# Kernel tuning notes

Measured on AMD Instinct MI355X. Metric: run time of the kernel, lower is better.

## Reference

```python
import jax, jax.numpy as jnp
import numpy as np

B, N, C, H = 32, 384, 768, 12
EPS = 1e-6

def setup_inputs() -> dict:
    key = jax.random.key(0)
    k0, k1, k2, k3 = jax.random.split(key, 4)
    x = jax.random.normal(k0, (B, N, C), dtype=jnp.float32)
    # binary keep-mask over key tokens, broadcastable to [B,1,N,N]
    policy = (jax.random.uniform(k1, (B, 1, 1, N)) > 0.5).astype(jnp.float32)
    qkv_w = jax.random.normal(k2, (3 * C, C), dtype=jnp.float32) * 0.02
    qkv_b = jnp.zeros((3 * C,), dtype=jnp.float32)
    proj_w = jax.random.normal(k3, (C, C), dtype=jnp.float32) * 0.02
    proj_b = jnp.zeros((C,), dtype=jnp.float32)
    return {"x": x, "policy": policy, "qkv_w": qkv_w, "qkv_b": qkv_b,
            "proj_w": proj_w, "proj_b": proj_b}

def reference(x, policy, qkv_w, qkv_b, proj_w, proj_b):
    b, n, c = x.shape
    hd = c // H
    scale = hd ** -0.5
    qkv = (x @ qkv_w.T + qkv_b).reshape(b, n, 3, H, hd).transpose(2, 0, 3, 1, 4)
    q, k, v = qkv[0], qkv[1], qkv[2]
    attn = jnp.einsum('bhnd,bhmd->bhnm', q, k) * scale  # [B,H,N,N]
    # softmax_with_policy: eye-blend so every token attends to itself,
    # then eps-regularized masked softmax
    eye = jnp.eye(n, dtype=policy.dtype)[None, None]  # [1,1,N,N]
    attn_policy = policy + (1.0 - policy) * eye       # broadcast -> [B,1,N,N]
    max_att = attn.max(axis=-1, keepdims=True)
    e = jnp.exp(attn - max_att) * attn_policy
    attn = (e + EPS / n) / (e.sum(axis=-1, keepdims=True) + EPS)
    out = jnp.einsum('bhnm,bhmd->bnhd', attn, v).reshape(b, n, c)
    return out @ proj_w.T + proj_b
```

## Files before the change

kernel.cpp:

```cpp
#include <hip/hip_runtime.h>

#define BB 32
#define NN 384
#define CC 768
#define HH 12
#define HD 64

typedef __attribute__((ext_vector_type(4))) float f32x4;
typedef __attribute__((ext_vector_type(8))) __bf16 bf16x8;
typedef __attribute__((ext_vector_type(4))) __bf16 bf16x4;

static __device__ __forceinline__ f32x4 mfma16(bf16x8 a, bf16x8 b, f32x4 c) {
    return __builtin_amdgcn_mfma_f32_16x16x32_bf16(a, b, c, 0, 0, 0);
}

__global__ void cvt_kernel(const float* __restrict__ src, __bf16* __restrict__ dst,
                           int n8, float scale) {
    int i = blockIdx.x * blockDim.x + threadIdx.x;
    if (i >= n8) return;
    f32x4 a = *(const f32x4*)(src + (size_t)i * 8);
    f32x4 b = *(const f32x4*)(src + (size_t)i * 8 + 4);
    bf16x8 o;
#pragma unroll
    for (int j = 0; j < 4; ++j) { o[j] = (__bf16)(a[j] * scale); o[j + 4] = (__bf16)(b[j] * scale); }
    *(bf16x8*)(dst + (size_t)i * 8) = o;
}

template <int EPI>
__global__ __launch_bounds__(256, 2) void gemm_kernel(
    const __bf16* __restrict__ A, const __bf16* __restrict__ Bw,
    const float* __restrict__ bias,
    __bf16* __restrict__ qkbuf, __bf16* __restrict__ vtbuf,
    float* __restrict__ fout) {
    __shared__ __bf16 Alds[128][72];
    __shared__ __bf16 Blds[128][72];

    const int tid = threadIdx.x;
    const int l = tid & 63;
    const int w = tid >> 6;
    const int g = l >> 4, q16 = l & 15;
    const int mb = blockIdx.x * 128;
    const int nb = blockIdx.y * 128;
    const int wrb = (w >> 1) * 64;
    const int wcb = (w & 1) * 64;
    const int srow = tid >> 3;
    const int sc8 = (tid & 7) * 8;

    const __bf16* Ab = A + (size_t)mb * CC;
    const __bf16* Bb = Bw + (size_t)nb * CC;

    f32x4 acc[4][4] = {};
    bf16x8 sa[4], sb[4];

#pragma unroll
    for (int p = 0; p < 4; ++p) {
        sa[p] = *(const bf16x8*)&Ab[(size_t)(p * 32 + srow) * CC + sc8];
        sb[p] = *(const bf16x8*)&Bb[(size_t)(p * 32 + srow) * CC + sc8];
    }

    for (int kt = 0; kt < 12; ++kt) {
#pragma unroll
        for (int p = 0; p < 4; ++p) {
            *(bf16x8*)&Alds[p * 32 + srow][sc8] = sa[p];
            *(bf16x8*)&Blds[p * 32 + srow][sc8] = sb[p];
        }
        __syncthreads();
        if (kt < 11) {
            const int kn = (kt + 1) * 64 + sc8;
#pragma unroll
            for (int p = 0; p < 4; ++p) {
                sa[p] = *(const bf16x8*)&Ab[(size_t)(p * 32 + srow) * CC + kn];
                sb[p] = *(const bf16x8*)&Bb[(size_t)(p * 32 + srow) * CC + kn];
            }
        }
#pragma unroll
        for (int c = 0; c < 2; ++c) {
            bf16x8 af[4], bf_[4];
#pragma unroll
            for (int m = 0; m < 4; ++m)
                af[m] = *(const bf16x8*)&Alds[wrb + m * 16 + q16][c * 32 + g * 8];
#pragma unroll
            for (int n = 0; n < 4; ++n)
                bf_[n] = *(const bf16x8*)&Blds[wcb + n * 16 + q16][c * 32 + g * 8];
#pragma unroll
            for (int m = 0; m < 4; ++m)
#pragma unroll
                for (int n = 0; n < 4; ++n)
                    acc[m][n] = mfma16(af[m], bf_[n], acc[m][n]);
        }
        __syncthreads();
    }

    if constexpr (EPI == 0) {
        const int bbatch = mb / NN;
        const int tokb = mb % NN;
#pragma unroll
        for (int n = 0; n < 4; ++n) {
            const int colb = nb + wcb + n * 16;
            const int col = colb + q16;
            float bs = bias[col];
            if (colb < 2 * CC) {
                if (colb < CC) bs *= 0.125f;
#pragma unroll
                for (int m = 0; m < 4; ++m) {
                    const int row = mb + wrb + m * 16 + g * 4;
#pragma unroll
                    for (int r = 0; r < 4; ++r)
                        qkbuf[(size_t)(row + r) * 1536 + col] = (__bf16)(acc[m][n][r] + bs);
                }
            } else {
                const int dd = (col - 2 * CC) & 63;
                const int hh = (colb - 2 * CC) >> 6;
                __bf16* vp = vtbuf + ((size_t)(bbatch * HH + hh) * HD + dd) * NN;
#pragma unroll
                for (int m = 0; m < 4; ++m) {
                    const int tok = tokb + wrb + m * 16 + g * 4;
                    bf16x4 pk;
#pragma unroll
                    for (int r = 0; r < 4; ++r) pk[r] = (__bf16)(acc[m][n][r] + bs);
                    *(bf16x4*)&vp[tok] = pk;
                }
            }
        }
    } else {
#pragma unroll
        for (int n = 0; n < 4; ++n) {
            const int col = nb + wcb + n * 16 + q16;
            const float bs = bias[col];
#pragma unroll
            for (int m = 0; m < 4; ++m)
#pragma unroll
                for (int r = 0; r < 4; ++r)
                    fout[(size_t)(mb + wrb + m * 16 + g * 4 + r) * CC + col] = acc[m][n][r] + bs;
        }
    }
}

__global__ __launch_bounds__(512, 2) void attn_kernel(
    const __bf16* __restrict__ qkbuf, const __bf16* __restrict__ vtbuf,
    const float* __restrict__ policy, __bf16* __restrict__ attb) {
    __shared__ __bf16 Klds[NN][72];
    __shared__ __bf16 Vlds[HD][NN + 8];
    __shared__ float pol[NN];

    const int tid = threadIdx.x;
    const int l = tid & 63;
    const int w = tid >> 6;
    const int g = l >> 4, q16 = l & 15;
    const int qblk = blockIdx.x;
    const int h = blockIdx.y;
    const int b = blockIdx.z;

    if (tid < NN) pol[tid] = policy[b * NN + tid];

    const __bf16* kg = qkbuf + (size_t)b * NN * 1536 + CC + h * HD;
#pragma unroll
    for (int p = 0; p < 6; ++p) {
        const int s = p * 512 + tid;
        const int row = s >> 3, c8 = (s & 7) * 8;
        *(bf16x8*)&Klds[row][c8] = *(const bf16x8*)&kg[(size_t)row * 1536 + c8];
    }
    const __bf16* vg = vtbuf + (size_t)(b * HH + h) * HD * NN;
#pragma unroll
    for (int p = 0; p < 6; ++p) {
        const int s = p * 512 + tid;
        const int d = s / 48, tk = (s % 48) * 8;
        *(bf16x8*)&Vlds[d][tk] = *(const bf16x8*)&vg[(size_t)s * 8];
    }
    __syncthreads();

    const int qrow = qblk * 128 + w * 16 + q16;
    const __bf16* qg = qkbuf + ((size_t)b * NN + qrow) * 1536 + h * HD;
    bf16x8 qf0 = *(const bf16x8*)&qg[g * 8];
    bf16x8 qf1 = *(const bf16x8*)&qg[32 + g * 8];

    f32x4 st[24];
#pragma unroll
    for (int t = 0; t < 24; ++t) {
        bf16x8 k0 = *(const bf16x8*)&Klds[t * 16 + q16][g * 8];
        bf16x8 k1 = *(const bf16x8*)&Klds[t * 16 + q16][32 + g * 8];
        f32x4 z = {0.f, 0.f, 0.f, 0.f};
        st[t] = mfma16(k1, qf1, mfma16(k0, qf0, z));
    }

    float mx = -1e30f;
#pragma unroll
    for (int t = 0; t < 24; ++t)
#pragma unroll
        for (int r = 0; r < 4; ++r) mx = fmaxf(mx, st[t][r]);
    mx = fmaxf(mx, __shfl_xor(mx, 16));
    mx = fmaxf(mx, __shfl_xor(mx, 32));

    float sum = 0.f;
#pragma unroll
    for (int t = 0; t < 24; ++t) {
#pragma unroll
        for (int r = 0; r < 4; ++r) {
            const int key = t * 16 + g * 4 + r;
            const bool keep = (pol[key] > 0.5f) || (key == qrow);
            const float e = keep ? __expf(st[t][r] - mx) : 0.f;
            st[t][r] = e;
            sum += e;
        }
    }
    sum += __shfl_xor(sum, 16);
    sum += __shfl_xor(sum, 32);
    const float dinv = 1.f / (sum + 1e-6f);

    f32x4 oacc[4] = {};
#pragma unroll
    for (int c = 0; c < 12; ++c) {
        bf16x8 pf;
#pragma unroll
        for (int r = 0; r < 4; ++r) {
            pf[r] = (__bf16)st[2 * c][r];
            pf[r + 4] = (__bf16)st[2 * c + 1][r];
        }
#pragma unroll
        for (int db = 0; db < 4; ++db) {
            bf16x4 v0 = *(const bf16x4*)&Vlds[db * 16 + q16][c * 32 + g * 4];
            bf16x4 v1 = *(const bf16x4*)&Vlds[db * 16 + q16][c * 32 + 16 + g * 4];
            bf16x8 vf;
#pragma unroll
            for (int r = 0; r < 4; ++r) { vf[r] = v0[r]; vf[r + 4] = v1[r]; }
            oacc[db] = mfma16(vf, pf, oacc[db]);
        }
    }

    __bf16* op = attb + ((size_t)b * NN + qrow) * CC + h * HD;
#pragma unroll
    for (int db = 0; db < 4; ++db) {
        bf16x4 pk;
#pragma unroll
        for (int r = 0; r < 4; ++r) pk[r] = (__bf16)(oacc[db][r] * dinv);
        *(bf16x4*)&op[db * 16 + g * 4] = pk;
    }
}

extern "C" void kernel_launch(void* const* d_in, const int* in_sizes, int n_in,
                              void* d_out, int out_size, void* d_ws, size_t ws_size,
                              hipStream_t stream) {
    (void)in_sizes; (void)n_in; (void)out_size; (void)ws_size;
    const float* x      = (const float*)d_in[0];
    const float* policy = (const float*)d_in[1];
    const float* qkv_w  = (const float*)d_in[2];
    const float* qkv_b  = (const float*)d_in[3];
    const float* proj_w = (const float*)d_in[4];
    const float* proj_b = (const float*)d_in[5];
    float* out = (float*)d_out;

    __bf16* xb    = (__bf16*)d_ws;
    __bf16* wqkv  = xb + (size_t)12288 * 768;
    __bf16* wproj = wqkv + (size_t)2304 * 768;
    __bf16* qkbuf = wproj + (size_t)768 * 768;
    __bf16* vtbuf = qkbuf + (size_t)12288 * 1536;
    __bf16* attb  = vtbuf + (size_t)BB * HH * HD * NN;

    auto cvt = [&](const float* s, __bf16* d, size_t n, float sc) {
        const int n8 = (int)(n / 8);
        cvt_kernel<<<(n8 + 255) / 256, 256, 0, stream>>>(s, d, n8, sc);
    };
    cvt(x, xb, (size_t)12288 * 768, 1.f);
    cvt(qkv_w, wqkv, (size_t)768 * 768, 0.125f);
    cvt(qkv_w + (size_t)768 * 768, wqkv + (size_t)768 * 768, (size_t)1536 * 768, 1.f);
    cvt(proj_w, wproj, (size_t)768 * 768, 1.f);

    gemm_kernel<0><<<dim3(96, 18), 256, 0, stream>>>(xb, wqkv, qkv_b, qkbuf, vtbuf, nullptr);
    attn_kernel<<<dim3(3, HH, BB), 512, 0, stream>>>(qkbuf, vtbuf, policy, attb);
    gemm_kernel<1><<<dim3(96, 6), 256, 0, stream>>>(attb, wproj, proj_b, nullptr, nullptr, out);
}
```

Before: 155.1 us.

## Use direct global-to-LDS loads in GEMM and attention, read K from global

The GEMM now stages A/B tiles with global_load_lds straight into unpadded LDS. This drops the register prefetch double-buffering and raises the occupancy hint to 3. The attention kernel uses 256-thread blocks over 64 query rows, loads V into XOR-swizzled LDS via global_load_lds, reads K directly from global memory instead of LDS, and raises wave priority around the MFMA loops. The goal is to cut LDS footprint and staging instructions to raise occupancy. The cost is losing the global-load/compute overlap in the GEMM and adding repeated K reads from global/L2. Unpadded GEMM LDS rows may cause bank conflicts.

```diff
diff --git a/kernel.cpp b/kernel.cpp
--- a/kernel.cpp
+++ b/kernel.cpp
@@ -12,6 +12,11 @@
 
 static __device__ __forceinline__ f32x4 mfma16(bf16x8 a, bf16x8 b, f32x4 c) {
     return __builtin_amdgcn_mfma_f32_16x16x32_bf16(a, b, c, 0, 0, 0);
+}
+
+static __device__ __forceinline__ void gload_lds16(const void* g, void* l) {
+    __builtin_amdgcn_global_load_lds((const __attribute__((address_space(1))) void*)g,
+                                     (__attribute__((address_space(3))) void*)l, 16, 0, 0);
 }
 
 __global__ void cvt_kernel(const float* __restrict__ src, __bf16* __restrict__ dst,
@@ -27,13 +32,13 @@
 }
 
 template <int EPI>
-__global__ __launch_bounds__(256, 2) void gemm_kernel(
+__global__ __launch_bounds__(256, 3) void gemm_kernel(
     const __bf16* __restrict__ A, const __bf16* __restrict__ Bw,
     const float* __restrict__ bias,
     __bf16* __restrict__ qkbuf, __bf16* __restrict__ vtbuf,
     float* __restrict__ fout) {
-    __shared__ __bf16 Alds[128][72];
-    __shared__ __bf16 Blds[128][72];
+    __shared__ __bf16 Alds[128 * 64];
+    __shared__ __bf16 Blds[128 * 64];
 
     const int tid = threadIdx.x;
     const int l = tid & 63;
@@ -43,50 +48,34 @@
     const int nb = blockIdx.y * 128;
     const int wrb = (w >> 1) * 64;
     const int wcb = (w & 1) * 64;
-    const int srow = tid >> 3;
-    const int sc8 = (tid & 7) * 8;
-
-    const __bf16* Ab = A + (size_t)mb * CC;
-    const __bf16* Bb = Bw + (size_t)nb * CC;
+
+    const int srow = w * 8 + (l >> 3);
+    const int scol = (l & 7) * 8;
 
     f32x4 acc[4][4] = {};
-    bf16x8 sa[4], sb[4];
-
-#pragma unroll
-    for (int p = 0; p < 4; ++p) {
-        sa[p] = *(const bf16x8*)&Ab[(size_t)(p * 32 + srow) * CC + sc8];
-        sb[p] = *(const bf16x8*)&Bb[(size_t)(p * 32 + srow) * CC + sc8];
-    }
 
     for (int kt = 0; kt < 12; ++kt) {
-#pragma unroll
-        for (int p = 0; p < 4; ++p) {
-            *(bf16x8*)&Alds[p * 32 + srow][sc8] = sa[p];
-            *(bf16x8*)&Blds[p * 32 + srow][sc8] = sb[p];
+        const int kof = kt * 64 + scol;
+#pragma unroll
+        for (int i = 0; i < 4; ++i) {
+            gload_lds16(&A[(size_t)(mb + i * 32 + srow) * CC + kof], &Alds[i * 2048 + w * 512]);
+            gload_lds16(&Bw[(size_t)(nb + i * 32 + srow) * CC + kof], &Blds[i * 2048 + w * 512]);
         }
         __syncthreads();
-        if (kt < 11) {
-            const int kn = (kt + 1) * 64 + sc8;
-#pragma unroll
-            for (int p = 0; p < 4; ++p) {
-                sa[p] = *(const bf16x8*)&Ab[(size_t)(p * 32 + srow) * CC + kn];
-                sb[p] = *(const bf16x8*)&Bb[(size_t)(p * 32 + srow) * CC + kn];
-            }
-        }
 #pragma unroll
         for (int c = 0; c < 2; ++c) {
-            bf16x8 af[4], bf_[4];
+            bf16x8 af[4], bfr[4];
 #pragma unroll
             for (int m = 0; m < 4; ++m)
-                af[m] = *(const bf16x8*)&Alds[wrb + m * 16 + q16][c * 32 + g * 8];
+                af[m] = *(const bf16x8*)&Alds[(wrb + m * 16 + q16) * 64 + c * 32 + g * 8];
 #pragma unroll
             for (int n = 0; n < 4; ++n)
-                bf_[n] = *(const bf16x8*)&Blds[wcb + n * 16 + q16][c * 32 + g * 8];
+                bfr[n] = *(const bf16x8*)&Blds[(wcb + n * 16 + q16) * 64 + c * 32 + g * 8];
 #pragma unroll
             for (int m = 0; m < 4; ++m)
 #pragma unroll
                 for (int n = 0; n < 4; ++n)
-                    acc[m][n] = mfma16(af[m], bf_[n], acc[m][n]);
+                    acc[m][n] = mfma16(af[m], bfr[n], acc[m][n]);
         }
         __syncthreads();
     }
@@ -136,11 +125,10 @@
     }
 }
 
-__global__ __launch_bounds__(512, 2) void attn_kernel(
+__global__ __launch_bounds__(256, 3) void attn_kernel(
     const __bf16* __restrict__ qkbuf, const __bf16* __restrict__ vtbuf,
     const float* __restrict__ policy, __bf16* __restrict__ attb) {
-    __shared__ __bf16 Klds[NN][72];
-    __shared__ __bf16 Vlds[HD][NN + 8];
+    __shared__ __bf16 Vlds[HD * NN];
     __shared__ float pol[NN];
 
     const int tid = threadIdx.x;
@@ -151,37 +139,34 @@
     const int h = blockIdx.y;
     const int b = blockIdx.z;
 
-    if (tid < NN) pol[tid] = policy[b * NN + tid];
-
-    const __bf16* kg = qkbuf + (size_t)b * NN * 1536 + CC + h * HD;
-#pragma unroll
-    for (int p = 0; p < 6; ++p) {
-        const int s = p * 512 + tid;
-        const int row = s >> 3, c8 = (s & 7) * 8;
-        *(bf16x8*)&Klds[row][c8] = *(const bf16x8*)&kg[(size_t)row * 1536 + c8];
-    }
     const __bf16* vg = vtbuf + (size_t)(b * HH + h) * HD * NN;
 #pragma unroll
-    for (int p = 0; p < 6; ++p) {
-        const int s = p * 512 + tid;
-        const int d = s / 48, tk = (s % 48) * 8;
-        *(bf16x8*)&Vlds[d][tk] = *(const bf16x8*)&vg[(size_t)s * 8];
-    }
-    __syncthreads();
-
-    const int qrow = qblk * 128 + w * 16 + q16;
+    for (int p = 0; p < 12; ++p) {
+        const int cs = p * 256 + w * 64 + l;
+        const int row = cs / 48, cin = cs - row * 48;
+        gload_lds16(&vg[row * NN + ((cin ^ (row & 7)) << 3)], &Vlds[(p * 256 + w * 64) * 8]);
+    }
+    for (int i = tid; i < NN; i += 256) pol[i] = policy[b * NN + i];
+
+    const int qrow = qblk * 64 + w * 16 + q16;
     const __bf16* qg = qkbuf + ((size_t)b * NN + qrow) * 1536 + h * HD;
     bf16x8 qf0 = *(const bf16x8*)&qg[g * 8];
     bf16x8 qf1 = *(const bf16x8*)&qg[32 + g * 8];
 
+    const __bf16* kg = qkbuf + (size_t)b * NN * 1536 + CC + h * HD;
     f32x4 st[24];
+    __builtin_amdgcn_s_setprio(1);
 #pragma unroll
     for (int t = 0; t < 24; ++t) {
-        bf16x8 k0 = *(const bf16x8*)&Klds[t * 16 + q16][g * 8];
-        bf16x8 k1 = *(const bf16x8*)&Klds[t * 16 + q16][32 + g * 8];
+        const __bf16* kr = &kg[(size_t)(t * 16 + q16) * 1536 + g * 8];
+        bf16x8 k0 = *(const bf16x8*)kr;
+        bf16x8 k1 = *(const bf16x8*)(kr + 32);
         f32x4 z = {0.f, 0.f, 0.f, 0.f};
         st[t] = mfma16(k1, qf1, mfma16(k0, qf0, z));
     }
+    __builtin_amdgcn_s_setprio(0);
+
+    __syncthreads();
 
     float mx = -1e30f;
 #pragma unroll
@@ -208,6 +193,7 @@
     const float dinv = 1.f / (sum + 1e-6f);
 
     f32x4 oacc[4] = {};
+    __builtin_amdgcn_s_setprio(1);
 #pragma unroll
     for (int c = 0; c < 12; ++c) {
         bf16x8 pf;
@@ -218,14 +204,18 @@
         }
 #pragma unroll
         for (int db = 0; db < 4; ++db) {
-            bf16x4 v0 = *(const bf16x4*)&Vlds[db * 16 + q16][c * 32 + g * 4];
-            bf16x4 v1 = *(const bf16x4*)&Vlds[db * 16 + q16][c * 32 + 16 + g * 4];
+            const int row = db * 16 + q16;
+            const int sw = (row & 7) << 4;
+            const int byte0 = (row * NN + c * 32 + g * 4) * 2;
+            bf16x4 v0 = *(const bf16x4*)((const char*)Vlds + (byte0 ^ sw));
+            bf16x4 v1 = *(const bf16x4*)((const char*)Vlds + ((byte0 + 32) ^ sw));
             bf16x8 vf;
 #pragma unroll
             for (int r = 0; r < 4; ++r) { vf[r] = v0[r]; vf[r + 4] = v1[r]; }
             oacc[db] = mfma16(vf, pf, oacc[db]);
         }
     }
+    __builtin_amdgcn_s_setprio(0);
 
     __bf16* op = attb + ((size_t)b * NN + qrow) * CC + h * HD;
 #pragma unroll
@@ -266,6 +256,6 @@
     cvt(proj_w, wproj, (size_t)768 * 768, 1.f);
 
     gemm_kernel<0><<<dim3(96, 18), 256, 0, stream>>>(xb, wqkv, qkv_b, qkbuf, vtbuf, nullptr);
-    attn_kernel<<<dim3(3, HH, BB), 512, 0, stream>>>(qkbuf, vtbuf, policy, attb);
+    attn_kernel<<<dim3(6, HH, BB), 256, 0, stream>>>(qkbuf, vtbuf, policy, attb);
     gemm_kernel<1><<<dim3(96, 6), 256, 0, stream>>>(attb, wproj, proj_b, nullptr, nullptr, out);
 }
```

Measured after the change: 178.2 us. 14.9% more time.
